# Kernel tuning notes

Hardware: AMD Instinct MI355X
Metric: run time of the kernel (lower is better)

## Reference

```python
import jax, jax.numpy as jnp
import numpy as np

T, H, I = 8192, 4096, 11008  # tokens, hidden, intermediate (LLaMA-7B)


def setup_inputs() -> dict:
    key = jax.random.key(0)
    ks = jax.random.split(key, 8)
    # int8-valued tensors stored as int32 (spec dtype enum lacks int8)
    hidden_states = jax.random.randint(ks[0], (T, H), -128, 128, dtype=jnp.int32)
    gate_w = jax.random.randint(ks[1], (I, H), -128, 128, dtype=jnp.int32)
    up_w = jax.random.randint(ks[2], (I, H), -128, 128, dtype=jnp.int32)
    down_w = jax.random.randint(ks[3], (H, I), -128, 128, dtype=jnp.int32)
    # per-tensor dequant scales (alpha = input_scale * weight_scale); small so
    # the SwiGLU product lands roughly in int8 range before requantization
    gate_a = jnp.float32(0.004)
    up_a = jnp.float32(0.004)
    down_a = jnp.float32(0.004)
    gate_b = jax.random.normal(ks[4], (I,), dtype=jnp.float32)
    up_b = jax.random.normal(ks[5], (I,), dtype=jnp.float32)
    down_b = jax.random.normal(ks[6], (H,), dtype=jnp.float32)
    return dict(hidden_states=hidden_states, gate_w=gate_w, gate_a=gate_a,
                gate_b=gate_b, up_w=up_w, up_a=up_a, up_b=up_b,
                down_w=down_w, down_a=down_a, down_b=down_b)


def _w8a8_linear(x_i8, w_i8, alpha, bias):
    # scale alpha and fp32 bias (W8A8BFP32OFP32Linear semantics).
    acc = jnp.matmul(x_i8.astype(jnp.int8), w_i8.astype(jnp.int8).T,
                     preferred_element_type=jnp.int32)
    return acc.astype(jnp.float32) * alpha + bias


def reference(hidden_states, gate_w, gate_a, gate_b, up_w, up_a, up_b,
              down_w, down_a, down_b):
    x1 = jax.nn.silu(_w8a8_linear(hidden_states, gate_w, gate_a, gate_b))  # [T,I]
    x2 = _w8a8_linear(hidden_states, up_w, up_a, up_b)                     # [T,I]
    x = x1 * x2
    # requantize: round, clamp to int8 range
    q = jnp.clip(jnp.round(x), -128.0, 127.0).astype(jnp.int32)
    return _w8a8_linear(q, down_w, down_a, down_b)                          # [T,H]
```

## Files before the change

### kernel.cpp

```cpp
#include <hip/hip_runtime.h>
#include <math.h>

#define T_DIM 8192
#define H_DIM 4096
#define I_DIM 11008

typedef int v4i __attribute__((ext_vector_type(4)));

#define AS1(p) ((const __attribute__((address_space(1))) void*)(p))
#define AS3(p) ((__attribute__((address_space(3))) void*)(p))

#define WAIT_VM_BAR(N) asm volatile("s_waitcnt vmcnt(" #N ")\n\ts_barrier" ::: "memory")
#define BARRIER() __builtin_amdgcn_s_barrier()
#define LGKM0 do { asm volatile("s_waitcnt lgkmcnt(0)" ::: "memory"); \
                   __builtin_amdgcn_sched_barrier(0); } while (0)

__device__ __forceinline__ v4i DSR(const char* p) {
  v4i r;
  unsigned a = (unsigned)(size_t)(const __attribute__((address_space(3))) char*)p;
  asm volatile("ds_read_b128 %0, %1" : "=v"(r) : "v"(a));
  return r;
}

__global__ void pack_i8(const int* __restrict__ src, char* __restrict__ dst, long n16) {
  long i = (long)blockIdx.x * blockDim.x + threadIdx.x;
  long stride = (long)gridDim.x * blockDim.x;
  for (; i < n16; i += stride) {
    const int4* s = (const int4*)src + i * 4;
    int4 a = s[0], b = s[1], c = s[2], d = s[3];
    int w0 = (a.x & 255) | ((a.y & 255) << 8) | ((a.z & 255) << 16) | (a.w << 24);
    int w1 = (b.x & 255) | ((b.y & 255) << 8) | ((b.z & 255) << 16) | (b.w << 24);
    int w2 = (c.x & 255) | ((c.y & 255) << 8) | ((c.z & 255) << 16) | (c.w << 24);
    int w3 = (d.x & 255) | ((d.y & 255) << 8) | ((d.z & 255) << 16) | (d.w << 24);
    ((int4*)dst)[i] = make_int4(w0, w1, w2, w3);
  }
}

__global__ __launch_bounds__(512, 2) void gemm_gateup(
    const char* __restrict__ A, const char* __restrict__ Bg, const char* __restrict__ Bu,
    const float* __restrict__ ga_p, const float* __restrict__ gb,
    const float* __restrict__ ua_p, const float* __restrict__ ub,
    char* __restrict__ Q)
{
  __shared__ char lds[2][65536];
  const int tid = threadIdx.x;
  const int l = tid & 63;
  const int w = tid >> 6;
  const int wm = w >> 2, wn = w & 3;

  const int q8 = 2752 / 8;
  int bid = blockIdx.x;
  int wgid = (bid & 7) * q8 + (bid >> 3);
  int st = wgid >> 3, r = wgid & 7;
  int sm = st / 43, sn = st - sm * 43;
  const int m0 = (sm * 4 + (r & 3)) * 256;
  const int n0 = (sn * 2 + (r >> 2)) * 128;

  const v4i vz = {0, 0, 0, 0};
  v4i accg[8][2], accu[8][2];
#pragma unroll
  for (int i = 0; i < 8; ++i)
#pragma unroll
    for (int j = 0; j < 2; ++j) { accg[i][j] = vz; accu[i][j] = vz; }

  const int r8 = tid >> 3;
  const int gc = ((tid & 7) << 4) ^ ((r8 & 7) << 4);
  const char* pA0 = A  + (size_t)(m0 +       r8) * H_DIM + gc;
  const char* pA1 = A  + (size_t)(m0 +  64 + r8) * H_DIM + gc;
  const char* pA2 = A  + (size_t)(m0 + 128 + r8) * H_DIM + gc;
  const char* pA3 = A  + (size_t)(m0 + 192 + r8) * H_DIM + gc;
  const char* pG0 = Bg + (size_t)(n0 +       r8) * H_DIM + gc;
  const char* pG1 = Bg + (size_t)(n0 +  64 + r8) * H_DIM + gc;
  const char* pU0 = Bu + (size_t)(n0 +       r8) * H_DIM + gc;
  const char* pU1 = Bu + (size_t)(n0 +  64 + r8) * H_DIM + gc;
  const int dd = tid * 16;

#define STG(buf, src, k0, coff) \
  __builtin_amdgcn_global_load_lds(AS1((src) + (k0)), AS3((buf) + (coff) + dd), 16, 0, 0)

  const int kg = l >> 4, li = l & 15;
  int oA[2][8], oB[2][2];
#pragma unroll
  for (int kk = 0; kk < 2; ++kk) {
    int slot = ((kk * 4 + kg) ^ (li & 7)) << 4;
#pragma unroll
    for (int mi = 0; mi < 8; ++mi) oA[kk][mi] = (wm * 128 + mi * 16 + li) * 128 + slot;
#pragma unroll
    for (int ni = 0; ni < 2; ++ni) oB[kk][ni] = (wn * 32 + ni * 16 + li) * 128 + slot;
  }

  const int nk = H_DIM / 128;

  {
    char* B0 = lds[0];
    STG(B0, pA0, 0, 0);     STG(B0, pA2, 0, 16384); STG(B0, pG0, 0, 32768);
    STG(B0, pG1, 0, 40960); STG(B0, pU0, 0, 49152); STG(B0, pU1, 0, 57344);
    STG(B0, pA1, 0, 8192);  STG(B0, pA3, 0, 24576);
    WAIT_VM_BAR(2);
  }

#define GU4(mi, av)                                                                          \
  do {                                                                                       \
    accg[mi][0] = __builtin_amdgcn_mfma_i32_16x16x64_i8(av, gf0, accg[mi][0], 0, 0, 0);      \
    accu[mi][0] = __builtin_amdgcn_mfma_i32_16x16x64_i8(av, uf0, accu[mi][0], 0, 0, 0);      \
    accg[mi][1] = __builtin_amdgcn_mfma_i32_16x16x64_i8(av, gf1, accg[mi][1], 0, 0, 0);      \
    accu[mi][1] = __builtin_amdgcn_mfma_i32_16x16x64_i8(av, uf1, accu[mi][1], 0, 0, 0);      \
  } while (0)

  for (int t = 0; t < nk; ++t) {
    const char* L = lds[t & 1];
    char* SB = lds[(t & 1) ^ 1];
    const bool son = (t + 1) < nk;
    const int sk = (t + 1) * 128;

    {
      v4i gf0 = DSR(L + 32768 + oB[0][0]);
      v4i uf0 = DSR(L + 49152 + oB[0][0]);
      v4i gf1 = DSR(L + 32768 + oB[0][1]);
      v4i uf1 = DSR(L + 49152 + oB[0][1]);
      v4i a0 = DSR(L + oA[0][0]);
      v4i a1 = DSR(L + oA[0][1]);
      v4i a2 = DSR(L + oA[0][2]);
      v4i a3 = DSR(L + oA[0][3]);
      if (son) {
        STG(SB, pA0, sk, 0); STG(SB, pA2, sk, 16384); STG(SB, pG0, sk, 32768);
        WAIT_VM_BAR(3);
      } else {
        WAIT_VM_BAR(0);
      }
      LGKM0;
      __builtin_amdgcn_s_setprio(1);
      GU4(0, a0); GU4(1, a1); GU4(2, a2); GU4(3, a3);
      __builtin_amdgcn_s_setprio(0);
      BARRIER();
    }
    {
      v4i gf0 = DSR(L + 32768 + oB[0][0]);
      v4i uf0 = DSR(L + 49152 + oB[0][0]);
      v4i gf1 = DSR(L + 32768 + oB[0][1]);
      v4i uf1 = DSR(L + 49152 + oB[0][1]);
      v4i a4 = DSR(L + oA[0][4]);
      v4i a5 = DSR(L + oA[0][5]);
      v4i a6 = DSR(L + oA[0][6]);
      v4i a7 = DSR(L + oA[0][7]);
      if (son) { STG(SB, pG1, sk, 40960); STG(SB, pU0, sk, 49152); STG(SB, pU1, sk, 57344); }
      BARRIER();
      LGKM0;
      __builtin_amdgcn_s_setprio(1);
      GU4(4, a4); GU4(5, a5); GU4(6, a6); GU4(7, a7);
      __builtin_amdgcn_s_setprio(0);
      BARRIER();
    }
    {
      v4i gf0 = DSR(L + 32768 + oB[1][0]);
      v4i uf0 = DSR(L + 49152 + oB[1][0]);
      v4i gf1 = DSR(L + 32768 + oB[1][1]);
      v4i uf1 = DSR(L + 49152 + oB[1][1]);
      v4i a0 = DSR(L + oA[1][0]);
      v4i a1 = DSR(L + oA[1][1]);
      v4i a2 = DSR(L + oA[1][2]);
      v4i a3 = DSR(L + oA[1][3]);
      if (son) { STG(SB, pA1, sk, 8192); STG(SB, pA3, sk, 24576); }
      BARRIER();
      LGKM0;
      __builtin_amdgcn_s_setprio(1);
      GU4(0, a0); GU4(1, a1); GU4(2, a2); GU4(3, a3);
      __builtin_amdgcn_s_setprio(0);
      BARRIER();
    }
    {
      v4i gf0 = DSR(L + 32768 + oB[1][0]);
      v4i uf0 = DSR(L + 49152 + oB[1][0]);
      v4i gf1 = DSR(L + 32768 + oB[1][1]);
      v4i uf1 = DSR(L + 49152 + oB[1][1]);
      v4i a4 = DSR(L + oA[1][4]);
      v4i a5 = DSR(L + oA[1][5]);
      v4i a6 = DSR(L + oA[1][6]);
      v4i a7 = DSR(L + oA[1][7]);
      WAIT_VM_BAR(2);
      LGKM0;
      __builtin_amdgcn_s_setprio(1);
      GU4(4, a4); GU4(5, a5); GU4(6, a6); GU4(7, a7);
      __builtin_amdgcn_s_setprio(0);
      BARRIER();
    }
  }
#undef GU4

  const float ga = *ga_p, ua = *ua_p;
#pragma unroll
  for (int ni = 0; ni < 2; ++ni) {
    int col = n0 + wn * 32 + ni * 16 + li;
    float gbv = gb[col], ubv = ub[col];
#pragma unroll
    for (int mi = 0; mi < 8; ++mi) {
      int rowb = m0 + wm * 128 + mi * 16 + kg * 4;
#pragma unroll
      for (int rr = 0; rr < 4; ++rr) {
        float g = (float)accg[mi][ni][rr] * ga + gbv;
        float u = (float)accu[mi][ni][rr] * ua + ubv;
        float x1 = g / (1.0f + expf(-g));
        float x = rintf(x1 * u);
        x = fminf(fmaxf(x, -128.0f), 127.0f);
        Q[(size_t)(rowb + rr) * I_DIM + col] = (char)(int)x;
      }
    }
  }
}

__global__ __launch_bounds__(512, 2) void gemm_down(
    const char* __restrict__ Qm, const char* __restrict__ Bd,
    const float* __restrict__ da_p, const float* __restrict__ db,
    float* __restrict__ out)
{
  __shared__ char lds[2][65536];
  const int tid = threadIdx.x;
  const int l = tid & 63;
  const int w = tid >> 6;
  const int wm = w >> 2, wn = w & 3;

  const int q8 = 512 / 8;
  int bid = blockIdx.x;
  int wgid = (bid & 7) * q8 + (bid >> 3);
  int st = wgid >> 3, r = wgid & 7;
  int sm = st >> 3, sn = st & 7;
  const int m0 = (sm * 4 + (r & 3)) * 256;
  const int n0 = (sn * 2 + (r >> 2)) * 256;

  const v4i vz = {0, 0, 0, 0};
  v4i acc[8][4];
#pragma unroll
  for (int i = 0; i < 8; ++i)
#pragma unroll
    for (int j = 0; j < 4; ++j) acc[i][j] = vz;

  const int r8 = tid >> 3;
  const int gc = ((tid & 7) << 4) ^ ((r8 & 7) << 4);
  const char* pA0 = Qm + (size_t)(m0 +       r8) * I_DIM + gc;
  const char* pA1 = Qm + (size_t)(m0 +  64 + r8) * I_DIM + gc;
  const char* pA2 = Qm + (size_t)(m0 + 128 + r8) * I_DIM + gc;
  const char* pA3 = Qm + (size_t)(m0 + 192 + r8) * I_DIM + gc;
  const char* pB0 = Bd + (size_t)(n0 +       r8) * I_DIM + gc;
  const char* pB1 = Bd + (size_t)(n0 +  64 + r8) * I_DIM + gc;
  const char* pB2 = Bd + (size_t)(n0 + 128 + r8) * I_DIM + gc;
  const char* pB3 = Bd + (size_t)(n0 + 192 + r8) * I_DIM + gc;
  const int dd = tid * 16;

  const int kg = l >> 4, li = l & 15;
  int oA[2][8], oB[2][4];
#pragma unroll
  for (int kk = 0; kk < 2; ++kk) {
    int slot = ((kk * 4 + kg) ^ (li & 7)) << 4;
#pragma unroll
    for (int mi = 0; mi < 8; ++mi) oA[kk][mi] = (wm * 128 + mi * 16 + li) * 128 + slot;
#pragma unroll
    for (int ni = 0; ni < 4; ++ni) oB[kk][ni] = (wn * 64 + ni * 16 + li) * 128 + slot;
  }

  const int nk = I_DIM / 128;

  {
    char* B0 = lds[0];
    STG(B0, pA0, 0, 0);     STG(B0, pA2, 0, 16384); STG(B0, pB0, 0, 32768);
    STG(B0, pB1, 0, 40960); STG(B0, pB2, 0, 49152); STG(B0, pB3, 0, 57344);
    STG(B0, pA1, 0, 8192);  STG(B0, pA3, 0, 24576);
    WAIT_VM_BAR(2);
  }

#define DN4(mi, av)                                                                       \
  do {                                                                                    \
    acc[mi][0] = __builtin_amdgcn_mfma_i32_16x16x64_i8(av, bf0, acc[mi][0], 0, 0, 0);     \
    acc[mi][1] = __builtin_amdgcn_mfma_i32_16x16x64_i8(av, bf1, acc[mi][1], 0, 0, 0);     \
    acc[mi][2] = __builtin_amdgcn_mfma_i32_16x16x64_i8(av, bf2, acc[mi][2], 0, 0, 0);     \
    acc[mi][3] = __builtin_amdgcn_mfma_i32_16x16x64_i8(av, bf3, acc[mi][3], 0, 0, 0);     \
  } while (0)

  for (int t = 0; t < nk; ++t) {
    const char* L = lds[t & 1];
    char* SB = lds[(t & 1) ^ 1];
    const bool son = (t + 1) < nk;
    const int sk = (t + 1) * 128;

    {
      v4i bf0 = DSR(L + 32768 + oB[0][0]);
      v4i bf1 = DSR(L + 32768 + oB[0][1]);
      v4i bf2 = DSR(L + 32768 + oB[0][2]);
      v4i bf3 = DSR(L + 32768 + oB[0][3]);
      v4i a0 = DSR(L + oA[0][0]);
      v4i a1 = DSR(L + oA[0][1]);
      v4i a2 = DSR(L + oA[0][2]);
      v4i a3 = DSR(L + oA[0][3]);
      if (son) {
        STG(SB, pA0, sk, 0); STG(SB, pA2, sk, 16384); STG(SB, pB0, sk, 32768);
        WAIT_VM_BAR(3);
      } else {
        WAIT_VM_BAR(0);
      }
      LGKM0;
      __builtin_amdgcn_s_setprio(1);
      DN4(0, a0); DN4(1, a1); DN4(2, a2); DN4(3, a3);
      __builtin_amdgcn_s_setprio(0);
      BARRIER();
    }
    {
      v4i bf0 = DSR(L + 32768 + oB[0][0]);
      v4i bf1 = DSR(L + 32768 + oB[0][1]);
      v4i bf2 = DSR(L + 32768 + oB[0][2]);
      v4i bf3 = DSR(L + 32768 + oB[0][3]);
      v4i a4 = DSR(L + oA[0][4]);
      v4i a5 = DSR(L + oA[0][5]);
      v4i a6 = DSR(L + oA[0][6]);
      v4i a7 = DSR(L + oA[0][7]);
      if (son) { STG(SB, pB1, sk, 40960); STG(SB, pB2, sk, 49152); STG(SB, pB3, sk, 57344); }
      BARRIER();
      LGKM0;
      __builtin_amdgcn_s_setprio(1);
      DN4(4, a4); DN4(5, a5); DN4(6, a6); DN4(7, a7);
      __builtin_amdgcn_s_setprio(0);
      BARRIER();
    }
    {
      v4i bf0 = DSR(L + 32768 + oB[1][0]);
      v4i bf1 = DSR(L + 32768 + oB[1][1]);
      v4i bf2 = DSR(L + 32768 + oB[1][2]);
      v4i bf3 = DSR(L + 32768 + oB[1][3]);
      v4i a0 = DSR(L + oA[1][0]);
      v4i a1 = DSR(L + oA[1][1]);
      v4i a2 = DSR(L + oA[1][2]);
      v4i a3 = DSR(L + oA[1][3]);
      if (son) { STG(SB, pA1, sk, 8192); STG(SB, pA3, sk, 24576); }
      BARRIER();
      LGKM0;
      __builtin_amdgcn_s_setprio(1);
      DN4(0, a0); DN4(1, a1); DN4(2, a2); DN4(3, a3);
      __builtin_amdgcn_s_setprio(0);
      BARRIER();
    }
    {
      v4i bf0 = DSR(L + 32768 + oB[1][0]);
      v4i bf1 = DSR(L + 32768 + oB[1][1]);
      v4i bf2 = DSR(L + 32768 + oB[1][2]);
      v4i bf3 = DSR(L + 32768 + oB[1][3]);
      v4i a4 = DSR(L + oA[1][4]);
      v4i a5 = DSR(L + oA[1][5]);
      v4i a6 = DSR(L + oA[1][6]);
      v4i a7 = DSR(L + oA[1][7]);
      WAIT_VM_BAR(2);
      LGKM0;
      __builtin_amdgcn_s_setprio(1);
      DN4(4, a4); DN4(5, a5); DN4(6, a6); DN4(7, a7);
      __builtin_amdgcn_s_setprio(0);
      BARRIER();
    }
  }
#undef DN4

  const float da = *da_p;
#pragma unroll
  for (int ni = 0; ni < 4; ++ni) {
    int col = n0 + wn * 64 + ni * 16 + li;
    float dbv = db[col];
#pragma unroll
    for (int mi = 0; mi < 8; ++mi) {
      int rowb = m0 + wm * 128 + mi * 16 + kg * 4;
#pragma unroll
      for (int rr = 0; rr < 4; ++rr)
        out[(size_t)(rowb + rr) * H_DIM + col] = (float)acc[mi][ni][rr] * da + dbv;
    }
  }
}

extern "C" void kernel_launch(void* const* d_in, const int* in_sizes, int n_in,
                              void* d_out, int out_size, void* d_ws, size_t ws_size,
                              hipStream_t stream) {
  const int*   hs = (const int*)d_in[0];
  const int*   gw = (const int*)d_in[1];
  const float* ga = (const float*)d_in[2];
  const float* gb = (const float*)d_in[3];
  const int*   uw = (const int*)d_in[4];
  const float* ua = (const float*)d_in[5];
  const float* ub = (const float*)d_in[6];
  const int*   dw = (const int*)d_in[7];
  const float* da = (const float*)d_in[8];
  const float* db = (const float*)d_in[9];

  char* ws   = (char*)d_ws;
  char* hid8 = ws;
  char* g8   = hid8 + (size_t)T_DIM * H_DIM;
  char* u8   = g8   + (size_t)I_DIM * H_DIM;
  char* d8   = u8   + (size_t)I_DIM * H_DIM;
  char* q8   = d8   + (size_t)I_DIM * H_DIM;

  pack_i8<<<2048, 256, 0, stream>>>(hs, hid8, (long)T_DIM * H_DIM / 16);
  pack_i8<<<2048, 256, 0, stream>>>(gw, g8,   (long)I_DIM * H_DIM / 16);
  pack_i8<<<2048, 256, 0, stream>>>(uw, u8,   (long)I_DIM * H_DIM / 16);
  pack_i8<<<2048, 256, 0, stream>>>(dw, d8,   (long)I_DIM * H_DIM / 16);

  gemm_gateup<<<2752, 512, 0, stream>>>(hid8, g8, u8, ga, gb, ua, ub, q8);
  gemm_down<<<512, 512, 0, stream>>>(q8, d8, da, db, (float*)d_out);
}
```

Measured before the change: 1.153 ms.

## Switch both int8 GEMMs to 32x32x32 MFMA tiles with simplified staging schedule

Replaces the 16x16x64 int8 MFMA tiling with 32x32x32 MFMA instructions in both the gate/up and down GEMMs. It remaps LDS read offsets, accumulators and epilogue indexing to the 32x32 output layout, which cuts the number of ds_read_b128 fragment loads per MFMA. It also reorganises each k-step into four phases that issue loads grouped by A and B. The intermediate barriers are removed and replaced by a single full vmcnt(0) wait plus barrier at the end of each k-tile. This reduces LDS traffic and barrier count, but it gives up the finer-grained overlap of global-to-LDS loads with compute that the old staged waits provided.

```diff
diff --git a/kernel.cpp b/kernel.cpp
--- a/kernel.cpp
+++ b/kernel.cpp
@@ -5,13 +5,13 @@
 #define H_DIM 4096
 #define I_DIM 11008
 
-typedef int v4i __attribute__((ext_vector_type(4)));
+typedef int v4i  __attribute__((ext_vector_type(4)));
+typedef int v16i __attribute__((ext_vector_type(16)));
 
 #define AS1(p) ((const __attribute__((address_space(1))) void*)(p))
 #define AS3(p) ((__attribute__((address_space(3))) void*)(p))
 
 #define WAIT_VM_BAR(N) asm volatile("s_waitcnt vmcnt(" #N ")\n\ts_barrier" ::: "memory")
-#define BARRIER() __builtin_amdgcn_s_barrier()
 #define LGKM0 do { asm volatile("s_waitcnt lgkmcnt(0)" ::: "memory"); \
                    __builtin_amdgcn_sched_barrier(0); } while (0)
 
@@ -36,6 +36,9 @@
   }
 }
 
+#define STG(buf, src, k0, coff) \
+  __builtin_amdgcn_global_load_lds(AS1((src) + (k0)), AS3((buf) + (coff) + dd), 16, 0, 0)
+
 __global__ __launch_bounds__(512, 2) void gemm_gateup(
     const char* __restrict__ A, const char* __restrict__ Bg, const char* __restrict__ Bu,
     const float* __restrict__ ga_p, const float* __restrict__ gb,
@@ -56,12 +59,12 @@
   const int m0 = (sm * 4 + (r & 3)) * 256;
   const int n0 = (sn * 2 + (r >> 2)) * 128;
 
-  const v4i vz = {0, 0, 0, 0};
-  v4i accg[8][2], accu[8][2];
-#pragma unroll
-  for (int i = 0; i < 8; ++i)
-#pragma unroll
-    for (int j = 0; j < 2; ++j) { accg[i][j] = vz; accu[i][j] = vz; }
+  v16i accg[4], accu[4];
+#pragma unroll
+  for (int i = 0; i < 4; ++i) {
+#pragma unroll
+    for (int j = 0; j < 16; ++j) { accg[i][j] = 0; accu[i][j] = 0; }
+  }
 
   const int r8 = tid >> 3;
   const int gc = ((tid & 7) << 4) ^ ((r8 & 7) << 4);
@@ -75,36 +78,45 @@
   const char* pU1 = Bu + (size_t)(n0 +  64 + r8) * H_DIM + gc;
   const int dd = tid * 16;
 
-#define STG(buf, src, k0, coff) \
-  __builtin_amdgcn_global_load_lds(AS1((src) + (k0)), AS3((buf) + (coff) + dd), 16, 0, 0)
-
-  const int kg = l >> 4, li = l & 15;
-  int oA[2][8], oB[2][2];
-#pragma unroll
-  for (int kk = 0; kk < 2; ++kk) {
-    int slot = ((kk * 4 + kg) ^ (li & 7)) << 4;
-#pragma unroll
-    for (int mi = 0; mi < 8; ++mi) oA[kk][mi] = (wm * 128 + mi * 16 + li) * 128 + slot;
-#pragma unroll
-    for (int ni = 0; ni < 2; ++ni) oB[kk][ni] = (wn * 32 + ni * 16 + li) * 128 + slot;
+  const int li32 = l & 31, kg2 = l >> 5;
+  int oA[4][4], oB[4];
+#pragma unroll
+  for (int ks = 0; ks < 4; ++ks) {
+    int slot = (((ks * 2 + kg2) ^ (li32 & 7)) << 4);
+#pragma unroll
+    for (int mi = 0; mi < 4; ++mi) oA[ks][mi] = (wm * 128 + mi * 32 + li32) * 128 + slot;
+    oB[ks] = (wn * 32 + li32) * 128 + slot;
   }
 
   const int nk = H_DIM / 128;
 
   {
     char* B0 = lds[0];
-    STG(B0, pA0, 0, 0);     STG(B0, pA2, 0, 16384); STG(B0, pG0, 0, 32768);
-    STG(B0, pG1, 0, 40960); STG(B0, pU0, 0, 49152); STG(B0, pU1, 0, 57344);
-    STG(B0, pA1, 0, 8192);  STG(B0, pA3, 0, 24576);
-    WAIT_VM_BAR(2);
-  }
-
-#define GU4(mi, av)                                                                          \
-  do {                                                                                       \
-    accg[mi][0] = __builtin_amdgcn_mfma_i32_16x16x64_i8(av, gf0, accg[mi][0], 0, 0, 0);      \
-    accu[mi][0] = __builtin_amdgcn_mfma_i32_16x16x64_i8(av, uf0, accu[mi][0], 0, 0, 0);      \
-    accg[mi][1] = __builtin_amdgcn_mfma_i32_16x16x64_i8(av, gf1, accg[mi][1], 0, 0, 0);      \
-    accu[mi][1] = __builtin_amdgcn_mfma_i32_16x16x64_i8(av, uf1, accu[mi][1], 0, 0, 0);      \
+    STG(B0, pA0, 0, 0);     STG(B0, pA1, 0, 8192);  STG(B0, pA2, 0, 16384); STG(B0, pA3, 0, 24576);
+    STG(B0, pG0, 0, 32768); STG(B0, pG1, 0, 40960); STG(B0, pU0, 0, 49152); STG(B0, pU1, 0, 57344);
+    WAIT_VM_BAR(0);
+  }
+
+#define GUPH(ks, ...)                                                                    \
+  do {                                                                                   \
+    v4i gf = DSR(L + 32768 + oB[ks]);                                                    \
+    v4i uf = DSR(L + 49152 + oB[ks]);                                                    \
+    v4i a0 = DSR(L + oA[ks][0]);                                                         \
+    v4i a1 = DSR(L + oA[ks][1]);                                                         \
+    v4i a2 = DSR(L + oA[ks][2]);                                                         \
+    v4i a3 = DSR(L + oA[ks][3]);                                                         \
+    __VA_ARGS__                                                                          \
+    LGKM0;                                                                               \
+    __builtin_amdgcn_s_setprio(1);                                                       \
+    accg[0] = __builtin_amdgcn_mfma_i32_32x32x32_i8(a0, gf, accg[0], 0, 0, 0);           \
+    accu[0] = __builtin_amdgcn_mfma_i32_32x32x32_i8(a0, uf, accu[0], 0, 0, 0);           \
+    accg[1] = __builtin_amdgcn_mfma_i32_32x32x32_i8(a1, gf, accg[1], 0, 0, 0);           \
+    accu[1] = __builtin_amdgcn_mfma_i32_32x32x32_i8(a1, uf, accu[1], 0, 0, 0);           \
+    accg[2] = __builtin_amdgcn_mfma_i32_32x32x32_i8(a2, gf, accg[2], 0, 0, 0);           \
+    accu[2] = __builtin_amdgcn_mfma_i32_32x32x32_i8(a2, uf, accu[2], 0, 0, 0);           \
+    accg[3] = __builtin_amdgcn_mfma_i32_32x32x32_i8(a3, gf, accg[3], 0, 0, 0);           \
+    accu[3] = __builtin_amdgcn_mfma_i32_32x32x32_i8(a3, uf, accu[3], 0, 0, 0);           \
+    __builtin_amdgcn_s_setprio(0);                                                       \
   } while (0)
 
   for (int t = 0; t < nk; ++t) {
@@ -113,96 +125,33 @@
     const bool son = (t + 1) < nk;
     const int sk = (t + 1) * 128;
 
-    {
-      v4i gf0 = DSR(L + 32768 + oB[0][0]);
-      v4i uf0 = DSR(L + 49152 + oB[0][0]);
-      v4i gf1 = DSR(L + 32768 + oB[0][1]);
-      v4i uf1 = DSR(L + 49152 + oB[0][1]);
-      v4i a0 = DSR(L + oA[0][0]);
-      v4i a1 = DSR(L + oA[0][1]);
-      v4i a2 = DSR(L + oA[0][2]);
-      v4i a3 = DSR(L + oA[0][3]);
-      if (son) {
-        STG(SB, pA0, sk, 0); STG(SB, pA2, sk, 16384); STG(SB, pG0, sk, 32768);
-        WAIT_VM_BAR(3);
-      } else {
-        WAIT_VM_BAR(0);
-      }
-      LGKM0;
-      __builtin_amdgcn_s_setprio(1);
-      GU4(0, a0); GU4(1, a1); GU4(2, a2); GU4(3, a3);
-      __builtin_amdgcn_s_setprio(0);
-      BARRIER();
-    }
-    {
-      v4i gf0 = DSR(L + 32768 + oB[0][0]);
-      v4i uf0 = DSR(L + 49152 + oB[0][0]);
-      v4i gf1 = DSR(L + 32768 + oB[0][1]);
-      v4i uf1 = DSR(L + 49152 + oB[0][1]);
-      v4i a4 = DSR(L + oA[0][4]);
-      v4i a5 = DSR(L + oA[0][5]);
-      v4i a6 = DSR(L + oA[0][6]);
-      v4i a7 = DSR(L + oA[0][7]);
-      if (son) { STG(SB, pG1, sk, 40960); STG(SB, pU0, sk, 49152); STG(SB, pU1, sk, 57344); }
-      BARRIER();
-      LGKM0;
-      __builtin_amdgcn_s_setprio(1);
-      GU4(4, a4); GU4(5, a5); GU4(6, a6); GU4(7, a7);
-      __builtin_amdgcn_s_setprio(0);
-      BARRIER();
-    }
-    {
-      v4i gf0 = DSR(L + 32768 + oB[1][0]);
-      v4i uf0 = DSR(L + 49152 + oB[1][0]);
-      v4i gf1 = DSR(L + 32768 + oB[1][1]);
-      v4i uf1 = DSR(L + 49152 + oB[1][1]);
-      v4i a0 = DSR(L + oA[1][0]);
-      v4i a1 = DSR(L + oA[1][1]);
-      v4i a2 = DSR(L + oA[1][2]);
-      v4i a3 = DSR(L + oA[1][3]);
-      if (son) { STG(SB, pA1, sk, 8192); STG(SB, pA3, sk, 24576); }
-      BARRIER();
-      LGKM0;
-      __builtin_amdgcn_s_setprio(1);
-      GU4(0, a0); GU4(1, a1); GU4(2, a2); GU4(3, a3);
-      __builtin_amdgcn_s_setprio(0);
-      BARRIER();
-    }
-    {
-      v4i gf0 = DSR(L + 32768 + oB[1][0]);
-      v4i uf0 = DSR(L + 49152 + oB[1][0]);
-      v4i gf1 = DSR(L + 32768 + oB[1][1]);
-      v4i uf1 = DSR(L + 49152 + oB[1][1]);
-      v4i a4 = DSR(L + oA[1][4]);
-      v4i a5 = DSR(L + oA[1][5]);
-      v4i a6 = DSR(L + oA[1][6]);
-      v4i a7 = DSR(L + oA[1][7]);
-      WAIT_VM_BAR(2);
-      LGKM0;
-      __builtin_amdgcn_s_setprio(1);
-      GU4(4, a4); GU4(5, a5); GU4(6, a6); GU4(7, a7);
-      __builtin_amdgcn_s_setprio(0);
-      BARRIER();
-    }
-  }
-#undef GU4
+    GUPH(0, if (son) { STG(SB, pA0, sk, 0);     STG(SB, pA1, sk, 8192);
+                       STG(SB, pA2, sk, 16384); STG(SB, pA3, sk, 24576); });
+    GUPH(1, if (son) { STG(SB, pG0, sk, 32768); STG(SB, pG1, sk, 40960);
+                       STG(SB, pU0, sk, 49152); STG(SB, pU1, sk, 57344); });
+    GUPH(2, );
+    GUPH(3, );
+    WAIT_VM_BAR(0);
+  }
+#undef GUPH
 
   const float ga = *ga_p, ua = *ua_p;
-#pragma unroll
-  for (int ni = 0; ni < 2; ++ni) {
-    int col = n0 + wn * 32 + ni * 16 + li;
-    float gbv = gb[col], ubv = ub[col];
-#pragma unroll
-    for (int mi = 0; mi < 8; ++mi) {
-      int rowb = m0 + wm * 128 + mi * 16 + kg * 4;
+  const int col = n0 + wn * 32 + li32;
+  const float gbv = gb[col], ubv = ub[col];
+#pragma unroll
+  for (int mi = 0; mi < 4; ++mi) {
+    const int rowb = m0 + wm * 128 + mi * 32 + kg2 * 4;
+#pragma unroll
+    for (int rq = 0; rq < 4; ++rq) {
 #pragma unroll
       for (int rr = 0; rr < 4; ++rr) {
-        float g = (float)accg[mi][ni][rr] * ga + gbv;
-        float u = (float)accu[mi][ni][rr] * ua + ubv;
+        const int rg = rq * 4 + rr;
+        float g = (float)accg[mi][rg] * ga + gbv;
+        float u = (float)accu[mi][rg] * ua + ubv;
         float x1 = g / (1.0f + expf(-g));
         float x = rintf(x1 * u);
         x = fminf(fmaxf(x, -128.0f), 127.0f);
-        Q[(size_t)(rowb + rr) * I_DIM + col] = (char)(int)x;
+        Q[(size_t)(rowb + rq * 8 + rr) * I_DIM + col] = (char)(int)x;
       }
     }
   }
@@ -227,12 +176,15 @@
   const int m0 = (sm * 4 + (r & 3)) * 256;
   const int n0 = (sn * 2 + (r >> 2)) * 256;
 
-  const v4i vz = {0, 0, 0, 0};
-  v4i acc[8][4];
-#pragma unroll
-  for (int i = 0; i < 8; ++i)
-#pragma unroll
-    for (int j = 0; j < 4; ++j) acc[i][j] = vz;
+  v16i acc[4][2];
+#pragma unroll
+  for (int i = 0; i < 4; ++i) {
+#pragma unroll
+    for (int n = 0; n < 2; ++n) {
+#pragma unroll
+      for (int j = 0; j < 16; ++j) acc[i][n][j] = 0;
+    }
+  }
 
   const int r8 = tid >> 3;
   const int gc = ((tid & 7) << 4) ^ ((r8 & 7) << 4);
@@ -246,33 +198,46 @@
   const char* pB3 = Bd + (size_t)(n0 + 192 + r8) * I_DIM + gc;
   const int dd = tid * 16;
 
-  const int kg = l >> 4, li = l & 15;
-  int oA[2][8], oB[2][4];
-#pragma unroll
-  for (int kk = 0; kk < 2; ++kk) {
-    int slot = ((kk * 4 + kg) ^ (li & 7)) << 4;
-#pragma unroll
-    for (int mi = 0; mi < 8; ++mi) oA[kk][mi] = (wm * 128 + mi * 16 + li) * 128 + slot;
-#pragma unroll
-    for (int ni = 0; ni < 4; ++ni) oB[kk][ni] = (wn * 64 + ni * 16 + li) * 128 + slot;
+  const int li32 = l & 31, kg2 = l >> 5;
+  int oA[4][4], oB[4][2];
+#pragma unroll
+  for (int ks = 0; ks < 4; ++ks) {
+    int slot = (((ks * 2 + kg2) ^ (li32 & 7)) << 4);
+#pragma unroll
+    for (int mi = 0; mi < 4; ++mi) oA[ks][mi] = (wm * 128 + mi * 32 + li32) * 128 + slot;
+#pragma unroll
+    for (int ni = 0; ni < 2; ++ni) oB[ks][ni] = (wn * 64 + ni * 32 + li32) * 128 + slot;
   }
 
   const int nk = I_DIM / 128;
 
   {
     char* B0 = lds[0];
-    STG(B0, pA0, 0, 0);     STG(B0, pA2, 0, 16384); STG(B0, pB0, 0, 32768);
-    STG(B0, pB1, 0, 40960); STG(B0, pB2, 0, 49152); STG(B0, pB3, 0, 57344);
-    STG(B0, pA1, 0, 8192);  STG(B0, pA3, 0, 24576);
-    WAIT_VM_BAR(2);
-  }
-
-#define DN4(mi, av)                                                                       \
-  do {                                                                                    \
-    acc[mi][0] = __builtin_amdgcn_mfma_i32_16x16x64_i8(av, bf0, acc[mi][0], 0, 0, 0);     \
-    acc[mi][1] = __builtin_amdgcn_mfma_i32_16x16x64_i8(av, bf1, acc[mi][1], 0, 0, 0);     \
-    acc[mi][2] = __builtin_amdgcn_mfma_i32_16x16x64_i8(av, bf2, acc[mi][2], 0, 0, 0);     \
-    acc[mi][3] = __builtin_amdgcn_mfma_i32_16x16x64_i8(av, bf3, acc[mi][3], 0, 0, 0);     \
+    STG(B0, pA0, 0, 0);     STG(B0, pA1, 0, 8192);  STG(B0, pA2, 0, 16384); STG(B0, pA3, 0, 24576);
+    STG(B0, pB0, 0, 32768); STG(B0, pB1, 0, 40960); STG(B0, pB2, 0, 49152); STG(B0, pB3, 0, 57344);
+    WAIT_VM_BAR(0);
+  }
+
+#define DNPH(ks, ...)                                                                    \
+  do {                                                                                   \
+    v4i bf0 = DSR(L + 32768 + oB[ks][0]);                                                \
+    v4i bf1 = DSR(L + 32768 + oB[ks][1]);                                                \
+    v4i a0 = DSR(L + oA[ks][0]);                                                         \
+    v4i a1 = DSR(L + oA[ks][1]);                                                         \
+    v4i a2 = DSR(L + oA[ks][2]);                                                         \
+    v4i a3 = DSR(L + oA[ks][3]);                                                         \
+    __VA_ARGS__                                                                          \
+    LGKM0;                                                                               \
+    __builtin_amdgcn_s_setprio(1);                                                       \
+    acc[0][0] = __builtin_amdgcn_mfma_i32_32x32x32_i8(a0, bf0, acc[0][0], 0, 0, 0);      \
+    acc[0][1] = __builtin_amdgcn_mfma_i32_32x32x32_i8(a0, bf1, acc[0][1], 0, 0, 0);      \
+    acc[1][0] = __builtin_amdgcn_mfma_i32_32x32x32_i8(a1, bf0, acc[1][0], 0, 0, 0);      \
+    acc[1][1] = __builtin_amdgcn_mfma_i32_32x32x32_i8(a1, bf1, acc[1][1], 0, 0, 0);      \
+    acc[2][0] = __builtin_amdgcn_mfma_i32_32x32x32_i8(a2, bf0, acc[2][0], 0, 0, 0);      \
+    acc[2][1] = __builtin_amdgcn_mfma_i32_32x32x32_i8(a2, bf1, acc[2][1], 0, 0, 0);      \
+    acc[3][0] = __builtin_amdgcn_mfma_i32_32x32x32_i8(a3, bf0, acc[3][0], 0, 0, 0);      \
+    acc[3][1] = __builtin_amdgcn_mfma_i32_32x32x32_i8(a3, bf1, acc[3][1], 0, 0, 0);      \
+    __builtin_amdgcn_s_setprio(0);                                                       \
   } while (0)
 
   for (int t = 0; t < nk; ++t) {
@@ -281,91 +246,31 @@
     const bool son = (t + 1) < nk;
     const int sk = (t + 1) * 128;
 
-    {
-      v4i bf0 = DSR(L + 32768 + oB[0][0]);
-      v4i bf1 = DSR(L + 32768 + oB[0][1]);
-      v4i bf2 = DSR(L + 32768 + oB[0][2]);
-      v4i bf3 = DSR(L + 32768 + oB[0][3]);
-      v4i a0 = DSR(L + oA[0][0]);
-      v4i a1 = DSR(L + oA[0][1]);
-      v4i a2 = DSR(L + oA[0][2]);
-      v4i a3 = DSR(L + oA[0][3]);
-      if (son) {
-        STG(SB, pA0, sk, 0); STG(SB, pA2, sk, 16384); STG(SB, pB0, sk, 32768);
-        WAIT_VM_BAR(3);
-      } else {
-        WAIT_VM_BAR(0);
+    DNPH(0, if (son) { STG(SB, pA0, sk, 0);     STG(SB, pA1, sk, 8192);
+                       STG(SB, pA2, sk, 16384); STG(SB, pA3, sk, 24576); });
+    DNPH(1, if (son) { STG(SB, pB0, sk, 32768); STG(SB, pB1, sk, 40960);
+                       STG(SB, pB2, sk, 49152); STG(SB, pB3, sk, 57344); });
+    DNPH(2, );
+    DNPH(3, );
+    WAIT_VM_BAR(0);
+  }
+#undef DNPH
+
+  const float da = *da_p;
+#pragma unroll
+  for (int ni = 0; ni < 2; ++ni) {
+    const int col = n0 + wn * 64 + ni * 32 + li32;
+    const float dbv = db[col];
+#pragma unroll
+    for (int mi = 0; mi < 4; ++mi) {
+      const int rowb = m0 + wm * 128 + mi * 32 + kg2 * 4;
+#pragma unroll
+      for (int rq = 0; rq < 4; ++rq) {
+#pragma unroll
+        for (int rr = 0; rr < 4; ++rr)
+          out[(size_t)(rowb + rq * 8 + rr) * H_DIM + col] =
+              (float)acc[mi][ni][rq * 4 + rr] * da + dbv;
       }
-      LGKM0;
-      __builtin_amdgcn_s_setprio(1);
-      DN4(0, a0); DN4(1, a1); DN4(2, a2); DN4(3, a3);
-      __builtin_amdgcn_s_setprio(0);
-      BARRIER();
-    }
-    {
-      v4i bf0 = DSR(L + 32768 + oB[0][0]);
-      v4i bf1 = DSR(L + 32768 + oB[0][1]);
-      v4i bf2 = DSR(L + 32768 + oB[0][2]);
-      v4i bf3 = DSR(L + 32768 + oB[0][3]);
-      v4i a4 = DSR(L + oA[0][4]);
-      v4i a5 = DSR(L + oA[0][5]);
-      v4i a6 = DSR(L + oA[0][6]);
-      v4i a7 = DSR(L + oA[0][7]);
-      if (son) { STG(SB, pB1, sk, 40960); STG(SB, pB2, sk, 49152); STG(SB, pB3, sk, 57344); }
-      BARRIER();
-      LGKM0;
-      __builtin_amdgcn_s_setprio(1);
-      DN4(4, a4); DN4(5, a5); DN4(6, a6); DN4(7, a7);
-      __builtin_amdgcn_s_setprio(0);
-      BARRIER();
-    }
-    {
-      v4i bf0 = DSR(L + 32768 + oB[1][0]);
-      v4i bf1 = DSR(L + 32768 + oB[1][1]);
-      v4i bf2 = DSR(L + 32768 + oB[1][2]);
-      v4i bf3 = DSR(L + 32768 + oB[1][3]);
-      v4i a0 = DSR(L + oA[1][0]);
-      v4i a1 = DSR(L + oA[1][1]);
-      v4i a2 = DSR(L + oA[1][2]);
-      v4i a3 = DSR(L + oA[1][3]);
-      if (son) { STG(SB, pA1, sk, 8192); STG(SB, pA3, sk, 24576); }
-      BARRIER();
-      LGKM0;
-      __builtin_amdgcn_s_setprio(1);
-      DN4(0, a0); DN4(1, a1); DN4(2, a2); DN4(3, a3);
-      __builtin_amdgcn_s_setprio(0);
-      BARRIER();
-    }
-    {
-      v4i bf0 = DSR(L + 32768 + oB[1][0]);
-      v4i bf1 = DSR(L + 32768 + oB[1][1]);
-      v4i bf2 = DSR(L + 32768 + oB[1][2]);
-      v4i bf3 = DSR(L + 32768 + oB[1][3]);
-      v4i a4 = DSR(L + oA[1][4]);
-      v4i a5 = DSR(L + oA[1][5]);
-      v4i a6 = DSR(L + oA[1][6]);
-      v4i a7 = DSR(L + oA[1][7]);
-      WAIT_VM_BAR(2);
-      LGKM0;
-      __builtin_amdgcn_s_setprio(1);
-      DN4(4, a4); DN4(5, a5); DN4(6, a6); DN4(7, a7);
-      __builtin_amdgcn_s_setprio(0);
-      BARRIER();
-    }
-  }
-#undef DN4
-
-  const float da = *da_p;
-#pragma unroll
-  for (int ni = 0; ni < 4; ++ni) {
-    int col = n0 + wn * 64 + ni * 16 + li;
-    float dbv = db[col];
-#pragma unroll
-    for (int mi = 0; mi < 8; ++mi) {
-      int rowb = m0 + wm * 128 + mi * 16 + kg * 4;
-#pragma unroll
-      for (int rr = 0; rr < 4; ++rr)
-        out[(size_t)(rowb + rr) * H_DIM + col] = (float)acc[mi][ni][rr] * da + dbv;
     }
   }
 }
```

Measured after the change: 1.164 ms. Within noise of the previous version (+0.9%).
